# Kernel optimization log

Measured on AMD Instinct MI355X. Metric: run time of the kernel, lower is better.

## Reference

```python
import jax, jax.numpy as jnp
import numpy as np

B, N, C, H, M = 32, 256, 1024, 16, 77
DH = C // H
W = int(N ** 0.5)
MLP_H = 4 * C

def _rel_index(w):
    ch = np.arange(w)
    coords = np.stack(np.meshgrid(ch, ch, indexing='ij'))  # [2, w, w]
    cf = coords.reshape(2, -1)
    rc = (cf[:, :, None] - cf[:, None, :]).transpose(1, 2, 0).astype(np.int64)
    rc[..., 0] += w - 1
    rc[..., 1] += w - 1
    rc[..., 0] *= 2 * w - 1
    return jnp.asarray(rc.sum(-1))  # [N, N]

REL_IDX = _rel_index(W)

def setup_inputs():
    key = jax.random.key(0)
    ks = jax.random.split(key, 12)
    p = lambda k, sh: jax.random.normal(k, sh, jnp.float32) * 0.02
    return dict(
        x=jax.random.normal(ks[0], (B, N, C), jnp.float32),
        noise_level=jax.random.normal(ks[1], (B, C), jnp.float32),
        y=jax.random.normal(ks[2], (B, M, C), jnp.float32),
        W_qkv=p(ks[3], (C, 3 * C)), b_qkv=jnp.zeros((3 * C,), jnp.float32),
        W_proj=p(ks[4], (C, C)), b_proj=jnp.zeros((C,), jnp.float32),
        rel_table=p(ks[5], ((2 * W - 1) ** 2 + 3, H)),
        W_ada=p(ks[6], (C, 6 * C)), b_ada=jnp.zeros((6 * C,), jnp.float32),
        W_fc1=p(ks[7], (C, MLP_H)), b_fc1=jnp.zeros((MLP_H,), jnp.float32),
        W_fc2=p(ks[8], (MLP_H, C)), b_fc2=jnp.zeros((C,), jnp.float32),
        W_q=p(ks[9], (C, C)), W_kv=p(ks[10], (C, 2 * C)),
    )

def _ln(x):
    # LayerNorm without affine, eps=1e-6, biased variance (matches torch)
    mu = x.mean(-1, keepdims=True)
    var = x.var(-1, keepdims=True)
    return (x - mu) * jax.lax.rsqrt(var + 1e-6)

def _modulate(x, shift, scale):
    return x * (1 + scale[:, None, :]) + shift[:, None, :]

def reference(x, noise_level, y, W_qkv, b_qkv, W_proj, b_proj, rel_table,
              W_ada, b_ada, W_fc1, b_fc1, W_fc2, b_fc2, W_q, W_kv):
    ada = jax.nn.silu(noise_level) @ W_ada + b_ada  # [B, 6C]
    sh_msa, sc_msa, g_msa, sh_mlp, sc_mlp, g_mlp = jnp.split(ada, 6, axis=1)

    # --- self-attention with relative position bias (heads split as (h d)) ---
    h = _modulate(_ln(x), sh_msa, sc_msa)
    qkv = (h @ W_qkv + b_qkv).reshape(B, N, 3, H, DH)
    q, k, v = qkv[:, :, 0], qkv[:, :, 1], qkv[:, :, 2]  # [B, N, H, DH]
    bias = rel_table[REL_IDX].transpose(2, 0, 1)  # [H, N, N]
    scores = jnp.einsum('bnhd,bmhd->bhnm', q, k) * (DH ** -0.5) + bias[None]
    attn = jax.nn.softmax(scores, axis=-1)
    o = jnp.einsum('bhnm,bmhd->bnhd', attn, v).reshape(B, N, C)
    x = x + g_msa[:, None, :] * (o @ W_proj + b_proj)

    # --- cross attention; einops '(d h)' split: head index is the FAST axis ---
    q2 = (x @ W_q).reshape(B, N, DH, H)
    kv = y @ W_kv
    k2 = kv[..., :C].reshape(B, M, DH, H)
    v2 = kv[..., C:].reshape(B, M, DH, H)
    s2 = jnp.einsum('bndh,bmdh->bhnm', q2, k2) * (DH ** -0.5)
    a2 = jax.nn.softmax(s2, axis=-1)
    o2 = jnp.einsum('bhnm,bmdh->bndh', a2, v2).reshape(B, N, C)
    x = x + o2

    # --- adaLN-modulated MLP with tanh-approx GELU ---
    h = _modulate(_ln(x), sh_mlp, sc_mlp)
    h = jax.nn.gelu(h @ W_fc1 + b_fc1, approximate=True) @ W_fc2 + b_fc2
    return x + g_mlp[:, None, :] * h
```

## Files before the change

kernel.cpp:

```cpp
#include <hip/hip_runtime.h>
#include <hip/hip_bf16.h>
#include <stdint.h>

typedef __hip_bfloat16 bf16;
using bf16x8 = __attribute__((ext_vector_type(8))) short;
using f32x4  = __attribute__((ext_vector_type(4))) float;


__device__ __forceinline__ void gload_lds16(const void* g, void* l) {
  using gchar = __attribute__((address_space(1))) char;
  using lchar = __attribute__((address_space(3))) char;
  gchar* gp = reinterpret_cast<gchar*>(reinterpret_cast<uintptr_t>(g));
  lchar* lp = reinterpret_cast<lchar*>(static_cast<uint32_t>(reinterpret_cast<uintptr_t>(l)));
  __builtin_amdgcn_global_load_lds(gp, lp, 16, 0, 0);
}

__device__ __forceinline__ unsigned short f2bf_bits(float x) {
  uint32_t u = __float_as_uint(x);
  uint32_t r = (u + 0x7fffu + ((u >> 16) & 1u)) >> 16;
  return (unsigned short)r;
}

template <int PERM>
__global__ __launch_bounds__(256) void transpose_bf16(
    const float* __restrict__ W, bf16* __restrict__ Wt, int K, int N) {
  __shared__ float t[32][33];
  const int n0 = blockIdx.x * 32, k0 = blockIdx.y * 32;
  const int tx = threadIdx.x & 31, ty = threadIdx.x >> 5;
  #pragma unroll
  for (int i = ty; i < 32; i += 8) t[i][tx] = W[(size_t)(k0 + i) * N + n0 + tx];
  __syncthreads();
  #pragma unroll
  for (int i = ty; i < 32; i += 8) {
    int n = n0 + i;
    int np;
    if constexpr (PERM == 0) np = n;
    else if constexpr (PERM == 1) np = (n & 15) * 64 + (n >> 4);
    else { int base = n & 1024, m = n & 1023; np = base + (m & 15) * 64 + (m >> 4); }
    Wt[(size_t)np * K + k0 + tx] = __float2bfloat16(t[tx][i]);
  }
}

__global__ __launch_bounds__(256) void conv_y(
    const float* __restrict__ y, bf16* __restrict__ yb) {
  int i = blockIdx.x * 256 + threadIdx.x;
  float v = (i < 2464 * 1024) ? y[i] : 0.f;
  yb[i] = __float2bfloat16(v);
}

__global__ __launch_bounds__(256) void silu_pad(
    const float* __restrict__ noise, bf16* __restrict__ Apad) {
  int i = blockIdx.x * 256 + threadIdx.x;
  float v = 0.f;
  if (i < 32 * 1024) {
    float x = noise[i];
    v = x / (1.f + __expf(-x));
  }
  Apad[i] = __float2bfloat16(v);
}

__global__ __launch_bounds__(256) void ln_mod(
    const float* __restrict__ x, const float* __restrict__ ada,
    int shOff, int scOff, bf16* __restrict__ out) {
  const int row = blockIdx.x, b = row >> 8, tid = threadIdx.x;
  const float* xr = x + (size_t)row * 1024;
  float v[4], s = 0.f, ss = 0.f;
  #pragma unroll
  for (int i = 0; i < 4; ++i) {
    v[i] = xr[tid + i * 256];
    s += v[i]; ss += v[i] * v[i];
  }
  #pragma unroll
  for (int o = 32; o; o >>= 1) { s += __shfl_xor(s, o); ss += __shfl_xor(ss, o); }
  __shared__ float red[8];
  const int w = tid >> 6;
  if ((tid & 63) == 0) { red[w] = s; red[w + 4] = ss; }
  __syncthreads();
  s = red[0] + red[1] + red[2] + red[3];
  ss = red[4] + red[5] + red[6] + red[7];
  float mu = s * (1.f / 1024.f);
  float var = ss * (1.f / 1024.f) - mu * mu;
  float rstd = rsqrtf(var + 1e-6f);
  const float* adab = ada + (size_t)b * 6144;
  #pragma unroll
  for (int i = 0; i < 4; ++i) {
    int c = tid + i * 256;
    float o = (v[i] - mu) * rstd * (1.f + adab[scOff + c]) + adab[shOff + c];
    out[(size_t)row * 1024 + c] = __float2bfloat16(o);
  }
}

enum { EPI_STORE = 0, EPI_GELU = 1, EPI_PROJ = 2, EPI_OUT = 3, EPI_ADAF = 4 };

template <int EPI>
__global__ __launch_bounds__(256, 2) void gemm_bf16(
    const bf16* __restrict__ A, const bf16* __restrict__ Bt,
    int N, int K, int gx, int grpG, int xcdP,
    const float* __restrict__ bias, const float* __restrict__ ada, int adaOff,
    const float* __restrict__ resid, float* __restrict__ outF,
    bf16* __restrict__ outB) {
  __shared__ bf16 As[128 * 64];
  __shared__ bf16 Bs[128 * 64];
  const int tid = threadIdx.x;
  const int w = tid >> 6, lane = tid & 63;
  const int wr = w >> 1, wc = w & 1;
  const int lr = lane >> 4, lc = lane & 15;

  const int flat = blockIdx.x;
  const int xcd = flat & 7, j = flat >> 3;
  const int cpg = gx / grpG;
  const int grp = xcd / xcdP, par = xcd % xcdP;
  const int bx = grp * cpg + j % cpg;
  const int by = (j / cpg) * xcdP + par;
  const int mBase = by * 128, nBase = bx * 128;

  f32x4 acc[4][4];
  #pragma unroll
  for (int mi = 0; mi < 4; ++mi)
    #pragma unroll
    for (int ni = 0; ni < 4; ++ni)
      #pragma unroll
      for (int j2 = 0; j2 < 4; ++j2) acc[mi][ni][j2] = 0.f;

  const int nK = K >> 6;
  for (int ks = 0; ks < nK; ++ks) {
    const int k0 = ks << 6;
    #pragma unroll
    for (int i = 0; i < 4; ++i) {
      int t16 = w * 256 + i * 64 + lane;
      int row = t16 >> 3;
      int cL = ((t16 & 7) ^ (row & 7)) << 3;
      gload_lds16(A + (size_t)(mBase + row) * K + k0 + cL, (char*)As + t16 * 16);
      gload_lds16(Bt + (size_t)(nBase + row) * K + k0 + cL, (char*)Bs + t16 * 16);
    }
    __syncthreads();
    #pragma unroll
    for (int kk = 0; kk < 2; ++kk) {
      bf16x8 af[4], bfr[4];
      #pragma unroll
      for (int mi = 0; mi < 4; ++mi) {
        int row = wr * 64 + mi * 16 + lc;
        int byte = row * 128 + ((kk * 64 + lr * 16) ^ ((row & 7) << 4));
        af[mi] = *reinterpret_cast<const bf16x8*>((const char*)As + byte);
      }
      #pragma unroll
      for (int ni = 0; ni < 4; ++ni) {
        int row = wc * 64 + ni * 16 + lc;
        int byte = row * 128 + ((kk * 64 + lr * 16) ^ ((row & 7) << 4));
        bfr[ni] = *reinterpret_cast<const bf16x8*>((const char*)Bs + byte);
      }
      #pragma unroll
      for (int mi = 0; mi < 4; ++mi)
        #pragma unroll
        for (int ni = 0; ni < 4; ++ni)
          acc[mi][ni] = __builtin_amdgcn_mfma_f32_16x16x32_bf16(
              af[mi], bfr[ni], acc[mi][ni], 0, 0, 0);
    }
    __syncthreads();
  }

  const int rB = mBase + wr * 64, cB = nBase + wc * 64;
  #pragma unroll
  for (int mi = 0; mi < 4; ++mi) {
    #pragma unroll
    for (int ni = 0; ni < 4; ++ni) {
      #pragma unroll
      for (int j2 = 0; j2 < 4; ++j2) {
        int r = rB + mi * 16 + lr * 4 + j2;
        int c = cB + ni * 16 + lc;
        float v = acc[mi][ni][j2];
        if (bias) v += bias[c];
        if constexpr (EPI == EPI_STORE) {
          outB[(size_t)r * N + c] = __float2bfloat16(v);
        } else if constexpr (EPI == EPI_GELU) {
          float e = __expf(1.5957691216057308f * v + 0.07135481627260086f * v * v * v);
          float t = 1.f - 2.f / (e + 1.f);
          outB[(size_t)r * N + c] = __float2bfloat16(0.5f * v * (1.f + t));
        } else if constexpr (EPI == EPI_PROJ) {
          int b = r >> 8;
          float g = ada[(size_t)b * 6144 + adaOff + c];
          float o = resid[(size_t)r * 1024 + c] + g * v;
          outF[(size_t)r * 1024 + c] = o;
          outB[(size_t)r * 1024 + c] = __float2bfloat16(o);
        } else if constexpr (EPI == EPI_OUT) {
          int b = r >> 8;
          float g = ada[(size_t)b * 6144 + adaOff + c];
          outF[(size_t)r * 1024 + c] = resid[(size_t)r * 1024 + c] + g * v;
        } else {
          if (r < 32) outF[(size_t)r * N + c] = v;
        }
      }
    }
  }
}

__global__ __launch_bounds__(512, 1) void attn1_mfma(
    const bf16* __restrict__ qkv, const float* __restrict__ rel,
    bf16* __restrict__ o) {
  __shared__ bf16 Ks[256 * 64];
  __shared__ bf16 Vt[64 * 256];
  __shared__ ushort Pl[8][32 * 40];
  __shared__ float bias_s[964];

  const int tid = threadIdx.x;
  const int w = tid >> 6, lane = tid & 63;
  const int p4 = lane >> 4, c = lane & 15;
  const int bh = blockIdx.x, b = bh >> 4, h = bh & 15;
  const bf16* basep = qkv + (size_t)b * 256 * 3072 + h * 64;

  #pragma unroll
  for (int it = 0; it < 4; ++it) {
    int t16 = it * 512 + tid;
    int row = t16 >> 3;
    int sc = ((t16 & 7) ^ (row & 7)) << 3;
    gload_lds16(basep + (size_t)row * 3072 + 1024 + sc, (char*)Ks + t16 * 16);
  }
  #pragma unroll
  for (int it = 0; it < 4; ++it) {
    int i = it * 512 + tid;
    int key = i >> 3, d0 = (i & 7) * 8;
    int4 u = *reinterpret_cast<const int4*>(basep + (size_t)key * 3072 + 2048 + d0);
    const ushort* us = reinterpret_cast<const ushort*>(&u);
    #pragma unroll
    for (int j = 0; j < 8; ++j) {
      int dh = d0 + j;
      int byte = dh * 512 + ((key * 2) ^ ((dh & 7) << 4));
      *reinterpret_cast<ushort*>((char*)Vt + byte) = us[j];
    }
  }
  for (int i = tid; i < 964; i += 512) bias_s[i] = rel[i * 16 + h];

  bf16x8 qf[2][2];
  #pragma unroll
  for (int mi = 0; mi < 2; ++mi)
    #pragma unroll
    for (int s = 0; s < 2; ++s) {
      int q = w * 32 + mi * 16 + c;
      int dh = s * 32 + p4 * 8;
      int4 u = *reinterpret_cast<const int4*>(basep + (size_t)q * 3072 + dh);
      uint32_t a[4] = {(uint32_t)u.x, (uint32_t)u.y, (uint32_t)u.z, (uint32_t)u.w};
      bf16x8 r;
      #pragma unroll
      for (int t = 0; t < 4; ++t) {
        float lo = __uint_as_float(a[t] << 16) * 0.125f;
        float hi = __uint_as_float(a[t] & 0xffff0000u) * 0.125f;
        r[2 * t]     = (short)(__float_as_uint(lo) >> 16);
        r[2 * t + 1] = (short)(__float_as_uint(hi) >> 16);
      }
      qf[mi][s] = r;
    }
  __syncthreads();

  float m_run[2][4], l_run[2][4];
  f32x4 oacc[2][4];
  #pragma unroll
  for (int mi = 0; mi < 2; ++mi)
    #pragma unroll
    for (int j = 0; j < 4; ++j) {
      m_run[mi][j] = -1e30f; l_run[mi][j] = 0.f;
      oacc[mi][j] = f32x4{0.f, 0.f, 0.f, 0.f};
    }

  ushort* Pw = &Pl[w][0];
  const int colterm = p4 * 4 - c + 15;

  for (int kt = 0; kt < 8; ++kt) {
    f32x4 sacc[2][2];
    #pragma unroll
    for (int mi = 0; mi < 2; ++mi)
      #pragma unroll
      for (int nf = 0; nf < 2; ++nf) {
        int bi = ((w * 2 + mi) - (kt * 2 + nf) + 15) * 31 + colterm;
        #pragma unroll
        for (int j = 0; j < 4; ++j) sacc[mi][nf][j] = bias_s[bi + j];
      }
    #pragma unroll
    for (int nf = 0; nf < 2; ++nf) {
      int key = kt * 32 + nf * 16 + c;
      #pragma unroll
      for (int s = 0; s < 2; ++s) {
        int byte = key * 128 + (((s * 4 + p4) ^ (key & 7)) << 4);
        bf16x8 kb = *reinterpret_cast<const bf16x8*>((const char*)Ks + byte);
        #pragma unroll
        for (int mi = 0; mi < 2; ++mi)
          sacc[mi][nf] = __builtin_amdgcn_mfma_f32_16x16x32_bf16(
              qf[mi][s], kb, sacc[mi][nf], 0, 0, 0);
      }
    }
    float sf[2][4];
    #pragma unroll
    for (int mi = 0; mi < 2; ++mi)
      #pragma unroll
      for (int j = 0; j < 4; ++j) {
        float cm = fmaxf(sacc[mi][0][j], sacc[mi][1][j]);
        cm = fmaxf(cm, __shfl_xor(cm, 1));
        cm = fmaxf(cm, __shfl_xor(cm, 2));
        cm = fmaxf(cm, __shfl_xor(cm, 4));
        cm = fmaxf(cm, __shfl_xor(cm, 8));
        float nm = fmaxf(m_run[mi][j], cm);
        sf[mi][j] = __expf(m_run[mi][j] - nm);
        m_run[mi][j] = nm;
        l_run[mi][j] *= sf[mi][j];
      }
    #pragma unroll
    for (int mi = 0; mi < 2; ++mi)
      #pragma unroll
      for (int nf = 0; nf < 4; ++nf)
        #pragma unroll
        for (int j = 0; j < 4; ++j) oacc[mi][nf][j] *= sf[mi][j];
    #pragma unroll
    for (int mi = 0; mi < 2; ++mi) {
      #pragma unroll
      for (int nf = 0; nf < 2; ++nf)
        #pragma unroll
        for (int j = 0; j < 4; ++j)
          sacc[mi][nf][j] = __expf(sacc[mi][nf][j] - m_run[mi][j]);
      #pragma unroll
      for (int j = 0; j < 4; ++j) {
        float lp = sacc[mi][0][j] + sacc[mi][1][j];
        lp += __shfl_xor(lp, 1);
        lp += __shfl_xor(lp, 2);
        lp += __shfl_xor(lp, 4);
        lp += __shfl_xor(lp, 8);
        l_run[mi][j] += lp;
      }
      #pragma unroll
      for (int nf = 0; nf < 2; ++nf)
        #pragma unroll
        for (int j = 0; j < 4; ++j)
          Pw[(mi * 16 + p4 * 4 + j) * 40 + nf * 16 + c] =
              f2bf_bits(sacc[mi][nf][j]);
    }
    bf16x8 pa[2], vb[4];
    #pragma unroll
    for (int mi = 0; mi < 2; ++mi)
      pa[mi] = *reinterpret_cast<const bf16x8*>(
          (const char*)Pw + (mi * 16 + c) * 80 + p4 * 16);
    #pragma unroll
    for (int nf = 0; nf < 4; ++nf) {
      int dh = nf * 16 + c;
      int byte = dh * 512 + (((kt * 4 + p4) ^ (dh & 7)) << 4);
      vb[nf] = *reinterpret_cast<const bf16x8*>((const char*)Vt + byte);
    }
    #pragma unroll
    for (int mi = 0; mi < 2; ++mi)
      #pragma unroll
      for (int nf = 0; nf < 4; ++nf)
        oacc[mi][nf] = __builtin_amdgcn_mfma_f32_16x16x32_bf16(
            pa[mi], vb[nf], oacc[mi][nf], 0, 0, 0);
  }

  #pragma unroll
  for (int mi = 0; mi < 2; ++mi) {
    float inv[4];
    #pragma unroll
    for (int j = 0; j < 4; ++j) inv[j] = 1.f / l_run[mi][j];
    #pragma unroll
    for (int nf = 0; nf < 4; ++nf)
      #pragma unroll
      for (int j = 0; j < 4; ++j) {
        int q = w * 32 + mi * 16 + p4 * 4 + j;
        int dh = nf * 16 + c;
        o[((size_t)b * 256 + q) * 1024 + h * 64 + dh] =
            __float2bfloat16(oacc[mi][nf][j] * inv[j]);
      }
  }
}

__global__ __launch_bounds__(512, 1) void attn2_mfma(
    const bf16* __restrict__ q2, const bf16* __restrict__ kv,
    bf16* __restrict__ o2) {
  __shared__ bf16 Ks[80 * 64];
  __shared__ bf16 Vt[64 * 128];
  __shared__ ushort Pl[8][32 * 104];

  const int tid = threadIdx.x;
  const int w = tid >> 6, lane = tid & 63;
  const int p4 = lane >> 4, c = lane & 15;
  const int bh = blockIdx.x, b = bh >> 4, h = bh & 15;
  const size_t kvrow0 = (size_t)b * 77;

  {
    int t16 = tid;
    int key = t16 >> 3;
    int sc = ((t16 & 7) ^ (key & 7)) << 3;
    gload_lds16(kv + (kvrow0 + key) * 2048 + h * 64 + sc, (char*)Ks + t16 * 16);
    if (tid < 128) {
      int u16 = 512 + tid; key = u16 >> 3;
      sc = ((u16 & 7) ^ (key & 7)) << 3;
      gload_lds16(kv + (kvrow0 + key) * 2048 + h * 64 + sc, (char*)Ks + u16 * 16);
    }
  }
  for (int i = tid; i < 80 * 8; i += 512) {
    int key = i >> 3, d0 = (i & 7) * 8;
    int4 u = *reinterpret_cast<const int4*>(
        kv + (kvrow0 + key) * 2048 + 1024 + h * 64 + d0);
    const ushort* us = reinterpret_cast<const ushort*>(&u);
    #pragma unroll
    for (int j = 0; j < 8; ++j) {
      int dh = d0 + j;
      int byte = dh * 256 + ((key * 2) ^ ((dh & 7) << 4));
      *reinterpret_cast<ushort*>((char*)Vt + byte) = us[j];
    }
  }
  {
    int row = lane >> 1, colb = 160 + (lane & 1) * 16;
    *reinterpret_cast<int4*>((char*)&Pl[w][0] + row * 208 + colb) =
        int4{0, 0, 0, 0};
  }
  bf16x8 qf[2][2];
  #pragma unroll
  for (int mi = 0; mi < 2; ++mi)
    #pragma unroll
    for (int s = 0; s < 2; ++s) {
      int q = w * 32 + mi * 16 + c;
      int dh = s * 32 + p4 * 8;
      int4 u = *reinterpret_cast<const int4*>(
          q2 + ((size_t)b * 256 + q) * 1024 + h * 64 + dh);
      uint32_t a[4] = {(uint32_t)u.x, (uint32_t)u.y, (uint32_t)u.z, (uint32_t)u.w};
      bf16x8 r;
      #pragma unroll
      for (int t = 0; t < 4; ++t) {
        float lo = __uint_as_float(a[t] << 16) * 0.125f;
        float hi = __uint_as_float(a[t] & 0xffff0000u) * 0.125f;
        r[2 * t]     = (short)(__float_as_uint(lo) >> 16);
        r[2 * t + 1] = (short)(__float_as_uint(hi) >> 16);
      }
      qf[mi][s] = r;
    }
  __syncthreads();

  f32x4 sacc[2][5];
  #pragma unroll
  for (int mi = 0; mi < 2; ++mi)
    #pragma unroll
    for (int nf = 0; nf < 5; ++nf)
      sacc[mi][nf] = f32x4{0.f, 0.f, 0.f, 0.f};
  #pragma unroll
  for (int nf = 0; nf < 5; ++nf) {
    int key = nf * 16 + c;
    #pragma unroll
    for (int s = 0; s < 2; ++s) {
      int byte = key * 128 + (((s * 4 + p4) ^ (key & 7)) << 4);
      bf16x8 kb = *reinterpret_cast<const bf16x8*>((const char*)Ks + byte);
      #pragma unroll
      for (int mi = 0; mi < 2; ++mi)
        sacc[mi][nf] = __builtin_amdgcn_mfma_f32_16x16x32_bf16(
            qf[mi][s], kb, sacc[mi][nf], 0, 0, 0);
    }
  }
  if (c >= 13) {
    #pragma unroll
    for (int mi = 0; mi < 2; ++mi)
      #pragma unroll
      for (int j = 0; j < 4; ++j) sacc[mi][4][j] = -1e30f;
  }
  float lrow[2][4];
  #pragma unroll
  for (int mi = 0; mi < 2; ++mi)
    #pragma unroll
    for (int j = 0; j < 4; ++j) {
      float cm = sacc[mi][0][j];
      #pragma unroll
      for (int nf = 1; nf < 5; ++nf) cm = fmaxf(cm, sacc[mi][nf][j]);
      cm = fmaxf(cm, __shfl_xor(cm, 1));
      cm = fmaxf(cm, __shfl_xor(cm, 2));
      cm = fmaxf(cm, __shfl_xor(cm, 4));
      cm = fmaxf(cm, __shfl_xor(cm, 8));
      float lp = 0.f;
      #pragma unroll
      for (int nf = 0; nf < 5; ++nf) {
        sacc[mi][nf][j] = __expf(sacc[mi][nf][j] - cm);
        lp += sacc[mi][nf][j];
      }
      lp += __shfl_xor(lp, 1);
      lp += __shfl_xor(lp, 2);
      lp += __shfl_xor(lp, 4);
      lp += __shfl_xor(lp, 8);
      lrow[mi][j] = lp;
    }
  ushort* Pw = &Pl[w][0];
  #pragma unroll
  for (int mi = 0; mi < 2; ++mi)
    #pragma unroll
    for (int nf = 0; nf < 5; ++nf)
      #pragma unroll
      for (int j = 0; j < 4; ++j)
        Pw[(mi * 16 + p4 * 4 + j) * 104 + nf * 16 + c] =
            f2bf_bits(sacc[mi][nf][j]);
  f32x4 oacc[2][4];
  #pragma unroll
  for (int mi = 0; mi < 2; ++mi)
    #pragma unroll
    for (int nf = 0; nf < 4; ++nf) oacc[mi][nf] = f32x4{0.f, 0.f, 0.f, 0.f};
  #pragma unroll
  for (int kk = 0; kk < 3; ++kk) {
    bf16x8 pa[2], vb[4];
    #pragma unroll
    for (int mi = 0; mi < 2; ++mi)
      pa[mi] = *reinterpret_cast<const bf16x8*>(
          (const char*)Pw + (mi * 16 + c) * 208 + kk * 64 + p4 * 16);
    #pragma unroll
    for (int nf = 0; nf < 4; ++nf) {
      int dh = nf * 16 + c;
      int byte = dh * 256 + (((kk * 4 + p4) ^ (dh & 7)) << 4);
      vb[nf] = *reinterpret_cast<const bf16x8*>((const char*)Vt + byte);
    }
    #pragma unroll
    for (int mi = 0; mi < 2; ++mi)
      #pragma unroll
      for (int nf = 0; nf < 4; ++nf)
        oacc[mi][nf] = __builtin_amdgcn_mfma_f32_16x16x32_bf16(
            pa[mi], vb[nf], oacc[mi][nf], 0, 0, 0);
  }
  #pragma unroll
  for (int mi = 0; mi < 2; ++mi) {
    float inv[4];
    #pragma unroll
    for (int j = 0; j < 4; ++j) inv[j] = 1.f / lrow[mi][j];
    #pragma unroll
    for (int nf = 0; nf < 4; ++nf)
      #pragma unroll
      for (int j = 0; j < 4; ++j) {
        int q = w * 32 + mi * 16 + p4 * 4 + j;
        int dh = nf * 16 + c;
        o2[((size_t)b * 256 + q) * 1024 + h * 64 + dh] =
            __float2bfloat16(oacc[mi][nf][j] * inv[j]);
      }
  }
}

__global__ __launch_bounds__(256) void permute_add(
    const bf16* __restrict__ o2, float* __restrict__ xcur) {
  __shared__ float s_lds[1088];
  const int tid = threadIdx.x;
  const int row0 = blockIdx.x * 4;
  for (int r = 0; r < 4; ++r) {
    const int row = row0 + r;
    #pragma unroll
    for (int i = 0; i < 4; ++i) {
      int cc = i * 256 + tid;
      float v = __bfloat162float(o2[(size_t)row * 1024 + cc]);
      s_lds[cc + (cc >> 4)] = v;
    }
    __syncthreads();
    float4 add;
    #pragma unroll
    for (int t = 0; t < 4; ++t) {
      int ct = tid * 4 + t;
      int src = (ct & 15) * 64 + (ct >> 4);
      (&add.x)[t] = s_lds[src + (src >> 4)];
    }
    float4* xp = reinterpret_cast<float4*>(xcur + (size_t)row * 1024 + tid * 4);
    float4 cur = *xp;
    cur.x += add.x; cur.y += add.y; cur.z += add.z; cur.w += add.w;
    *xp = cur;
    __syncthreads();
  }
}


extern "C" void kernel_launch(void* const* d_in, const int* in_sizes, int n_in,
                              void* d_out, int out_size, void* d_ws, size_t ws_size,
                              hipStream_t stream) {
  (void)in_sizes; (void)n_in; (void)out_size; (void)ws_size;
  const float* x      = (const float*)d_in[0];
  const float* noise  = (const float*)d_in[1];
  const float* y      = (const float*)d_in[2];
  const float* W_qkv  = (const float*)d_in[3];
  const float* b_qkv  = (const float*)d_in[4];
  const float* W_proj = (const float*)d_in[5];
  const float* b_proj = (const float*)d_in[6];
  const float* rel    = (const float*)d_in[7];
  const float* W_ada  = (const float*)d_in[8];
  const float* b_ada  = (const float*)d_in[9];
  const float* W_fc1  = (const float*)d_in[10];
  const float* b_fc1  = (const float*)d_in[11];
  const float* W_fc2  = (const float*)d_in[12];
  const float* b_fc2  = (const float*)d_in[13];
  const float* W_q    = (const float*)d_in[14];
  const float* W_kv   = (const float*)d_in[15];

  char* ws = (char*)d_ws;
  size_t off = 0;
  auto alloc = [&](size_t bytes) {
    char* p = ws + off;
    off = (off + bytes + 255) & ~(size_t)255;
    return p;
  };
  float* ada   = (float*)alloc(32u * 6144 * 4);
  float* xcur  = (float*)alloc(8192u * 1024 * 4);
  bf16* WqkvT  = (bf16*)alloc(3072u * 1024 * 2);
  bf16* WprojT = (bf16*)alloc(1024u * 1024 * 2);
  bf16* WqT    = (bf16*)alloc(1024u * 1024 * 2);
  bf16* WkvT   = (bf16*)alloc(2048u * 1024 * 2);
  bf16* Wfc1T  = (bf16*)alloc(4096u * 1024 * 2);
  bf16* Wfc2T  = (bf16*)alloc(1024u * 4096 * 2);
  bf16* WadaT  = (bf16*)alloc(6144u * 1024 * 2);
  bf16* Apad   = (bf16*)alloc(128u * 1024 * 2);
  bf16* hbuf   = (bf16*)alloc(8192u * 1024 * 2);
  bf16* big    = (bf16*)alloc(8192u * 4096 * 2);
  bf16* obuf   = (bf16*)alloc(8192u * 1024 * 2);
  bf16* kvbuf  = (bf16*)alloc(2560u * 2048 * 2);
  bf16* ybuf   = (bf16*)alloc(2560u * 1024 * 2);
  float* outF  = (float*)d_out;

  transpose_bf16<0><<<dim3(96, 32), 256, 0, stream>>>(W_qkv, WqkvT, 1024, 3072);
  transpose_bf16<0><<<dim3(32, 32), 256, 0, stream>>>(W_proj, WprojT, 1024, 1024);
  transpose_bf16<1><<<dim3(32, 32), 256, 0, stream>>>(W_q, WqT, 1024, 1024);
  transpose_bf16<2><<<dim3(64, 32), 256, 0, stream>>>(W_kv, WkvT, 1024, 2048);
  transpose_bf16<0><<<dim3(128, 32), 256, 0, stream>>>(W_fc1, Wfc1T, 1024, 4096);
  transpose_bf16<0><<<dim3(32, 128), 256, 0, stream>>>(W_fc2, Wfc2T, 4096, 1024);
  transpose_bf16<0><<<dim3(192, 32), 256, 0, stream>>>(W_ada, WadaT, 1024, 6144);
  conv_y<<<2560 * 1024 / 256, 256, 0, stream>>>(y, ybuf);

  silu_pad<<<512, 256, 0, stream>>>(noise, Apad);
  gemm_bf16<EPI_ADAF><<<48, 256, 0, stream>>>(
      Apad, WadaT, 6144, 1024, 48, 8, 1, b_ada, nullptr, 0, nullptr, ada, nullptr);

  ln_mod<<<8192, 256, 0, stream>>>(x, ada, 0, 1024, hbuf);
  gemm_bf16<EPI_STORE><<<1536, 256, 0, stream>>>(
      hbuf, WqkvT, 3072, 1024, 24, 4, 2, b_qkv, nullptr, 0, nullptr, nullptr, big);
  attn1_mfma<<<512, 512, 0, stream>>>(big, rel, obuf);
  gemm_bf16<EPI_PROJ><<<512, 256, 0, stream>>>(
      obuf, WprojT, 1024, 1024, 8, 1, 8, b_proj, ada, 2048, x, xcur, hbuf);

  gemm_bf16<EPI_STORE><<<512, 256, 0, stream>>>(
      hbuf, WqT, 1024, 1024, 8, 1, 8, nullptr, nullptr, 0, nullptr, nullptr, obuf);
  gemm_bf16<EPI_STORE><<<320, 256, 0, stream>>>(
      ybuf, WkvT, 2048, 1024, 16, 8, 1, nullptr, nullptr, 0, nullptr, nullptr, kvbuf);
  attn2_mfma<<<512, 512, 0, stream>>>(obuf, kvbuf, big);
  permute_add<<<2048, 256, 0, stream>>>(big, xcur);

  ln_mod<<<8192, 256, 0, stream>>>(xcur, ada, 3072, 4096, hbuf);
  gemm_bf16<EPI_GELU><<<2048, 256, 0, stream>>>(
      hbuf, Wfc1T, 4096, 1024, 32, 4, 2, b_fc1, nullptr, 0, nullptr, nullptr, big);
  gemm_bf16<EPI_OUT><<<512, 256, 0, stream>>>(
      big, Wfc2T, 1024, 4096, 8, 1, 8, b_fc2, ada, 5120, xcur, outF, nullptr);
}
```

Measured before the change: 536.5 us.

## Add 256x256-tile 512-thread GEMM for QKV and FC1 projections

Introduces a new GEMM kernel with 256x256 output tiles, 8 waves, double-buffered LDS staging via direct global-to-LDS loads with an XOR swizzle, and s_setprio around the MFMA block. The QKV and FC1 GEMMs switch to it with fewer, larger blocks. The aim is more operand reuse per LDS load and less global traffic per FLOP. In exchange it needs 128 KB of LDS and many accumulator registers, so only one block fits per CU and the grid is small (384 and 512 blocks over 256 CUs), which risks tail imbalance.

```diff
diff --git a/kernel.cpp b/kernel.cpp
--- a/kernel.cpp
+++ b/kernel.cpp
@@ -194,6 +194,128 @@
   }
 }
 
+template <int EPI>
+__global__ __launch_bounds__(512, 1) void gemm256_bf16(
+    const bf16* __restrict__ A, const bf16* __restrict__ Bt,
+    int N, int K, int gx, int grpG, int xcdP,
+    const float* __restrict__ bias, bf16* __restrict__ outB) {
+  __shared__ bf16 As[2 * 256 * 64];
+  __shared__ bf16 Bs[2 * 256 * 64];
+  const int tid = threadIdx.x;
+  const int w = tid >> 6, lane = tid & 63;
+  const int wr = w >> 2, wcn = w & 3;
+  const int lr = lane >> 4, lc = lane & 15;
+
+  const int flat = blockIdx.x;
+  const int xcd = flat & 7, jj = flat >> 3;
+  const int cpg = gx / grpG;
+  const int grp = xcd / xcdP, par = xcd % xcdP;
+  const int bx = grp * cpg + jj % cpg;
+  const int by = (jj / cpg) * xcdP + par;
+  const int mBase = by * 256, nBase = bx * 256;
+
+  f32x4 acc[8][4];
+  #pragma unroll
+  for (int mi = 0; mi < 8; ++mi)
+    #pragma unroll
+    for (int ni = 0; ni < 4; ++ni)
+      acc[mi][ni] = f32x4{0.f, 0.f, 0.f, 0.f};
+
+  const int nT = K >> 6;
+
+  auto STAGE = [&](int t, int bufI) {
+    const int k0 = t << 6;
+    char* Ad = (char*)As + bufI * 32768;
+    char* Bd = (char*)Bs + bufI * 32768;
+    #pragma unroll
+    for (int i = 0; i < 4; ++i) {
+      int ck = i * 512 + tid;
+      int row = ck >> 3;
+      int sc = ((ck & 7) ^ (row & 7)) << 3;
+      gload_lds16(A + (size_t)(mBase + row) * K + k0 + sc, Ad + ck * 16);
+      gload_lds16(Bt + (size_t)(nBase + row) * K + k0 + sc, Bd + ck * 16);
+    }
+  };
+
+  STAGE(0, 0);
+  STAGE(1, 1);
+  asm volatile("s_waitcnt vmcnt(8)" ::: "memory");
+  __builtin_amdgcn_sched_barrier(0);
+  __builtin_amdgcn_s_barrier();
+  __builtin_amdgcn_sched_barrier(0);
+
+  for (int t = 0; t < nT; ++t) {
+    const int cur = t & 1;
+    const char* Ab = (const char*)As + cur * 32768;
+    const char* Bb = (const char*)Bs + cur * 32768;
+    bf16x8 af[2][8], bfr[2][4];
+    #pragma unroll
+    for (int kk = 0; kk < 2; ++kk) {
+      #pragma unroll
+      for (int mi = 0; mi < 8; ++mi) {
+        int row = wr * 128 + mi * 16 + lc;
+        int byte = row * 128 + ((kk * 64 + lr * 16) ^ ((row & 7) << 4));
+        af[kk][mi] = *reinterpret_cast<const bf16x8*>(Ab + byte);
+      }
+      #pragma unroll
+      for (int ni = 0; ni < 4; ++ni) {
+        int row = wcn * 64 + ni * 16 + lc;
+        int byte = row * 128 + ((kk * 64 + lr * 16) ^ ((row & 7) << 4));
+        bfr[kk][ni] = *reinterpret_cast<const bf16x8*>(Bb + byte);
+      }
+    }
+    asm volatile("s_waitcnt lgkmcnt(0)" ::: "memory");
+    __builtin_amdgcn_sched_barrier(0);
+    __builtin_amdgcn_s_barrier();
+    __builtin_amdgcn_sched_barrier(0);
+
+    if (t + 2 < nT) STAGE(t + 2, cur);
+
+    __builtin_amdgcn_s_setprio(1);
+    #pragma unroll
+    for (int kk = 0; kk < 2; ++kk)
+      #pragma unroll
+      for (int mi = 0; mi < 8; ++mi)
+        #pragma unroll
+        for (int ni = 0; ni < 4; ++ni)
+          acc[mi][ni] = __builtin_amdgcn_mfma_f32_16x16x32_bf16(
+              af[kk][mi], bfr[kk][ni], acc[mi][ni], 0, 0, 0);
+    __builtin_amdgcn_s_setprio(0);
+
+    if (t < nT - 1) {
+      if (t + 2 < nT) {
+        asm volatile("s_waitcnt vmcnt(8)" ::: "memory");
+      } else {
+        asm volatile("s_waitcnt vmcnt(0)" ::: "memory");
+      }
+      __builtin_amdgcn_sched_barrier(0);
+      __builtin_amdgcn_s_barrier();
+      __builtin_amdgcn_sched_barrier(0);
+    }
+  }
+
+  const int rB = mBase + wr * 128, cB = nBase + wcn * 64;
+  #pragma unroll
+  for (int mi = 0; mi < 8; ++mi) {
+    #pragma unroll
+    for (int ni = 0; ni < 4; ++ni) {
+      #pragma unroll
+      for (int j2 = 0; j2 < 4; ++j2) {
+        int r = rB + mi * 16 + lr * 4 + j2;
+        int c = cB + ni * 16 + lc;
+        float v = acc[mi][ni][j2] + bias[c];
+        if constexpr (EPI == EPI_STORE) {
+          outB[(size_t)r * N + c] = __float2bfloat16(v);
+        } else {
+          float e = __expf(1.5957691216057308f * v + 0.07135481627260086f * v * v * v);
+          float t2 = 1.f - 2.f / (e + 1.f);
+          outB[(size_t)r * N + c] = __float2bfloat16(0.5f * v * (1.f + t2));
+        }
+      }
+    }
+  }
+}
+
 __global__ __launch_bounds__(512, 1) void attn1_mfma(
     const bf16* __restrict__ qkv, const float* __restrict__ rel,
     bf16* __restrict__ o) {
@@ -619,8 +741,8 @@
       Apad, WadaT, 6144, 1024, 48, 8, 1, b_ada, nullptr, 0, nullptr, ada, nullptr);
 
   ln_mod<<<8192, 256, 0, stream>>>(x, ada, 0, 1024, hbuf);
-  gemm_bf16<EPI_STORE><<<1536, 256, 0, stream>>>(
-      hbuf, WqkvT, 3072, 1024, 24, 4, 2, b_qkv, nullptr, 0, nullptr, nullptr, big);
+  gemm256_bf16<EPI_STORE><<<384, 512, 0, stream>>>(
+      hbuf, WqkvT, 3072, 1024, 12, 4, 2, b_qkv, big);
   attn1_mfma<<<512, 512, 0, stream>>>(big, rel, obuf);
   gemm_bf16<EPI_PROJ><<<512, 256, 0, stream>>>(
       obuf, WprojT, 1024, 1024, 8, 1, 8, b_proj, ada, 2048, x, xcur, hbuf);
@@ -633,8 +755,8 @@
   permute_add<<<2048, 256, 0, stream>>>(big, xcur);
 
   ln_mod<<<8192, 256, 0, stream>>>(xcur, ada, 3072, 4096, hbuf);
-  gemm_bf16<EPI_GELU><<<2048, 256, 0, stream>>>(
-      hbuf, Wfc1T, 4096, 1024, 32, 4, 2, b_fc1, nullptr, 0, nullptr, nullptr, big);
+  gemm256_bf16<EPI_GELU><<<512, 512, 0, stream>>>(
+      hbuf, Wfc1T, 4096, 1024, 16, 4, 2, b_fc1, big);
   gemm_bf16<EPI_OUT><<<512, 256, 0, stream>>>(
       big, Wfc2T, 1024, 4096, 8, 1, 8, b_fc2, ada, 5120, xcur, outF, nullptr);
 }
```

Result: faster. 518.1 us (-3.4%).
